# Optimization experiments

Measured on AMD Instinct MI355X. Metric: run time of the kernel, lower is better.

Reference implementation:

```python
import jax, jax.numpy as jnp
import numpy as np

NEG_SLOPE = 0.2

def gat_layer(x, src, dst, W, al, ar, b):
    # x: (N, F_in); W: (F_in, H*D); al/ar: (H, D); b: (H, D)
    N = x.shape[0]
    H, D = al.shape
    feat = (x @ W).reshape(N, H, D)                      # (N,H,D)
    el = jnp.sum(feat * al, axis=-1)                     # (N,H) src-side scores
    er = jnp.sum(feat * ar, axis=-1)                     # (N,H) dst-side scores
    e = jax.nn.leaky_relu(el[src] + er[dst], NEG_SLOPE)  # (E,H)
    # edge softmax over incoming edges of each dst node (numerically stable)
    m = jax.ops.segment_max(e, dst, num_segments=N)      # (N,H)
    m = jnp.where(jnp.isfinite(m), m, 0.0)               # guard isolated nodes
    ex = jnp.exp(e - m[dst])                             # (E,H)
    denom = jax.ops.segment_sum(ex, dst, num_segments=N) # (N,H)
    alpha = ex / jnp.maximum(denom[dst], 1e-30)          # (E,H)
    msg = alpha[:, :, None] * feat[src]                  # (E,H,D) gather + weight
    out = jax.ops.segment_sum(msg, dst, num_segments=N)  # (N,H,D) scatter-add
    return out + b[None]                                 # bias per head


def setup_inputs() -> dict:
    key = jax.random.key(0)
    ks = jax.random.split(key, 12)
    N, E, F_in, Dh = 100000, 1600000, 128, 64
    H1 = 2
    inp = {}
    inp['in_feat'] = jax.random.normal(ks[0], (N, F_in), dtype=jnp.float32)
    inp['src'] = jax.random.randint(ks[1], (E,), 0, N, dtype=jnp.int32)
    inp['dst'] = jax.random.randint(ks[2], (E,), 0, N, dtype=jnp.int32)
    s1 = 1.0 / np.sqrt(F_in)
    inp['W1'] = jax.random.normal(ks[3], (F_in, H1 * Dh), dtype=jnp.float32) * s1
    inp['al1'] = jax.random.normal(ks[4], (H1, Dh), dtype=jnp.float32) * 0.1
    inp['ar1'] = jax.random.normal(ks[5], (H1, Dh), dtype=jnp.float32) * 0.1
    inp['b1'] = jnp.zeros((H1, Dh), dtype=jnp.float32)
    s2 = 1.0 / np.sqrt(Dh)
    inp['W2'] = jax.random.normal(ks[6], (Dh, 1 * 2), dtype=jnp.float32) * s2
    inp['al2'] = jax.random.normal(ks[7], (1, 2), dtype=jnp.float32) * 0.1
    inp['ar2'] = jax.random.normal(ks[8], (1, 2), dtype=jnp.float32) * 0.1
    inp['b2'] = jnp.zeros((1, 2), dtype=jnp.float32)
    return inp


def reference(in_feat, src, dst, W1, al1, ar1, b1, W2, al2, ar2, b2):
    num_heads = al1.shape[0]
    h = gat_layer(in_feat, src, dst, W1, al1, ar1, b1)  # (N,2,64)
    h = jnp.sum(h, axis=1) / num_heads                  # head mean
    h = jax.nn.relu(h)
    out = gat_layer(h, src, dst, W2, al2, ar2, b2)      # (N,1,2)
    return out
```

## Files before the change

### kernel.cpp

```cpp
#include <hip/hip_runtime.h>
#include <hip/hip_bf16.h>
#include <hip/hip_fp16.h>

#define LEAKY 0.2f
#define NBMAX 1024
#define CCH   4096
#define SCAP2 3456

typedef _Float16 half8 __attribute__((ext_vector_type(8)));
typedef float f32x4 __attribute__((ext_vector_type(4)));

__device__ __forceinline__ float wave_sum64(float v) {
    #pragma unroll
    for (int m = 32; m > 0; m >>= 1) v += __shfl_xor(v, m, 64);
    return v;
}

__launch_bounds__(256)
__global__ void w1cvt_kernel(const float* __restrict__ W, __half* __restrict__ Wt) {
    int i = blockIdx.x * 256 + threadIdx.x;
    int n = i >> 7, k = i & 127;
    Wt[i] = __float2half(W[k * 128 + n]);
}

__launch_bounds__(256)
__global__ void gemm1_kernel(const float* __restrict__ X, const __half* __restrict__ Wt,
                             const float* __restrict__ al1, const float* __restrict__ ar1,
                             __half* __restrict__ feat_h,
                             float* __restrict__ el1, float* __restrict__ er1, int N) {
    __shared__ __half Al[64 * 136];
    __shared__ __half Wl[128 * 136];
    const int tid = threadIdx.x;
    const int r0 = blockIdx.x * 64;
    {
        int n = tid >> 1, h0 = (tid & 1) * 64;
        const __half* gsrc = Wt + n * 128 + h0;
        __half* ldst = Wl + n * 136 + h0;
        #pragma unroll
        for (int i = 0; i < 8; i++)
            *(uint4*)(ldst + i * 8) = *(const uint4*)(gsrc + i * 8);
    }
    {
        int r = tid >> 2, c0 = (tid & 3) * 32;
        int rr = r0 + r;
        const float* gsrc = X + (size_t)rr * 128 + c0;
        __half* ldst = Al + r * 136 + c0;
        if (rr < N) {
            #pragma unroll
            for (int i = 0; i < 8; i++) {
                float4 v = *(const float4*)(gsrc + i * 4);
                __half2 a = __floats2half2_rn(v.x, v.y);
                __half2 b = __floats2half2_rn(v.z, v.w);
                uint2 pk; pk.x = *(unsigned*)&a; pk.y = *(unsigned*)&b;
                *(uint2*)(ldst + i * 4) = pk;
            }
        } else {
            uint2 z; z.x = 0; z.y = 0;
            #pragma unroll
            for (int i = 0; i < 8; i++) *(uint2*)(ldst + i * 4) = z;
        }
    }
    __syncthreads();
    const int wv = tid >> 6, lane = tid & 63;
    const int lm = lane & 15, lq = lane >> 4;
    f32x4 acc[8];
    #pragma unroll
    for (int t = 0; t < 8; t++) acc[t] = (f32x4){0.f, 0.f, 0.f, 0.f};
    const __half* arow = Al + (wv * 16 + lm) * 136 + lq * 8;
    const __half* brow = Wl + lm * 136 + lq * 8;
    #pragma unroll
    for (int ks = 0; ks < 4; ks++) {
        half8 af = *(const half8*)(arow + ks * 32);
        #pragma unroll
        for (int nt = 0; nt < 8; nt++) {
            half8 bf = *(const half8*)(brow + nt * 16 * 136 + ks * 32);
            acc[nt] = __builtin_amdgcn_mfma_f32_16x16x32_f16(af, bf, acc[nt], 0, 0, 0);
        }
    }
    __syncthreads();
    __half* Cl = Al;
    #pragma unroll
    for (int nt = 0; nt < 8; nt++) {
        #pragma unroll
        for (int r = 0; r < 4; r++) {
            int m = wv * 16 + lq * 4 + r;
            Cl[m * 136 + nt * 16 + lm] = __float2half(acc[nt][r]);
        }
    }
    __syncthreads();
    {
        int r = tid >> 2, c0 = (tid & 3) * 32;
        int rr = r0 + r;
        float pel = 0.f, per = 0.f;
        const __half* crow = Cl + r * 136 + c0;
        if (rr < N) {
            #pragma unroll
            for (int i = 0; i < 4; i++)
                *(uint4*)(feat_h + (size_t)rr * 128 + c0 + i * 8) = *(const uint4*)(crow + i * 8);
            #pragma unroll
            for (int c = 0; c < 32; c++) {
                float fv = __half2float(crow[c]);
                pel += fv * al1[c0 + c];
                per += fv * ar1[c0 + c];
            }
        }
        pel += __shfl_xor(pel, 1, 64);
        per += __shfl_xor(per, 1, 64);
        if ((tid & 1) == 0 && rr < N) {
            int h = (tid >> 1) & 1;
            el1[rr * 2 + h] = pel;
            er1[rr * 2 + h] = per;
        }
    }
}

__launch_bounds__(256)
__global__ void bhist_kernel(const int* __restrict__ dst, int* __restrict__ bcount,
                             int E, int NB) {
    __shared__ int hls[NBMAX];
    for (int i = threadIdx.x; i < NB; i += 256) hls[i] = 0;
    __syncthreads();
    int stride = gridDim.x * 256;
    for (int e = blockIdx.x * 256 + threadIdx.x; e < E; e += stride)
        atomicAdd(&hls[dst[e] >> 7], 1);
    __syncthreads();
    for (int i = threadIdx.x; i < NB; i += 256) {
        int c = hls[i];
        if (c) atomicAdd(&bcount[i], c);
    }
}

__launch_bounds__(1024)
__global__ void bscan_kernel(const int* __restrict__ bcount, int* __restrict__ bstart,
                             int* __restrict__ bcursor, int NB) {
    __shared__ int sd[NBMAX];
    int t = threadIdx.x;
    int v = (t < NB) ? bcount[t] : 0;
    sd[t] = v;
    __syncthreads();
    for (int o = 1; o < NBMAX; o <<= 1) {
        int x = (t >= o) ? sd[t - o] : 0;
        __syncthreads();
        sd[t] += x;
        __syncthreads();
    }
    if (t < NB) { int ex = sd[t] - v; bstart[t] = ex; bcursor[t] = ex; }
}

__launch_bounds__(256)
__global__ void bscatter_kernel(const int* __restrict__ src, const int* __restrict__ dst,
                                const float* __restrict__ el1, const float* __restrict__ er1,
                                int* __restrict__ bcursor, uint2* __restrict__ erec,
                                int E, int NB) {
    __shared__ int hls[NBMAX];
    for (int i = threadIdx.x; i < NB; i += 256) hls[i] = 0;
    __syncthreads();
    const int b0 = blockIdx.x * CCH;
    uint2 ureg[16];
    int breg[16];
    #pragma unroll
    for (int k = 0; k < 16; k++) {
        int e = b0 + k * 256 + threadIdx.x;
        if (e < E) {
            int s = src[e], d = dst[e];
            int bk = d >> 7;
            breg[k] = bk;
            float2 lv = *((const float2*)el1 + s);
            float2 rv = *((const float2*)er1 + d);
            float e0 = lv.x + rv.x; e0 = (e0 > 0.f) ? e0 : LEAKY * e0;
            float e1 = lv.y + rv.y; e1 = (e1 > 0.f) ? e1 : LEAKY * e1;
            __half2 w = __floats2half2_rn(__expf(e0), __expf(e1));
            ureg[k].x = ((unsigned)s << 7) | (unsigned)(d & 127);
            ureg[k].y = *(unsigned*)&w;
            atomicAdd(&hls[bk], 1);
        } else breg[k] = -1;
    }
    __syncthreads();
    for (int b = threadIdx.x; b < NB; b += 256) {
        int c = hls[b];
        if (c) hls[b] = atomicAdd(&bcursor[b], c);
    }
    __syncthreads();
    #pragma unroll
    for (int k = 0; k < 16; k++) {
        if (breg[k] >= 0) {
            int p = atomicAdd(&hls[breg[k]], 1);
            erec[p] = ureg[k];
        }
    }
}

__launch_bounds__(256)
__global__ void bsort_kernel(const uint2* __restrict__ erec,
                             const int* __restrict__ bstart, const int* __restrict__ bcount,
                             uint2* __restrict__ erec2,
                             int* __restrict__ rowstart, int* __restrict__ plen,
                             int* __restrict__ tlen,
                             int N, int NB) {
    __shared__ uint2 sorted[SCAP2];
    __shared__ int cnt[128], prs[129], curs[128];
    const int tid = threadIdx.x;
    const int b = blockIdx.x;
    const int node0 = b << 7;
    const int nd = min(128, N - node0);
    const int ebase = bstart[b];
    int ecnt = bcount[b];
    if (ecnt > SCAP2 - 896) ecnt = SCAP2 - 896;
    const int pbase = ebase + 896 * b;
    if (tid < 128) cnt[tid] = 0;
    __syncthreads();
    for (int j = tid; j < ecnt; j += 256)
        atomicAdd(&cnt[erec[ebase + j].x & 127], 1);
    __syncthreads();
    int pv = 0;
    if (tid < 128) { pv = (cnt[tid] + 7) & ~7; curs[tid] = pv; }
    __syncthreads();
    for (int o = 1; o < 128; o <<= 1) {
        int x = 0;
        if (tid < 128 && tid >= o) x = curs[tid - o];
        __syncthreads();
        if (tid < 128) curs[tid] += x;
        __syncthreads();
    }
    if (tid < 128) prs[tid + 1] = curs[tid];
    if (tid == 0) prs[0] = 0;
    __syncthreads();
    if (tid < 128) curs[tid] = prs[tid + 1] - pv;
    __syncthreads();
    const int pecnt = prs[128];
    for (int j = tid; j < pecnt; j += 256) { sorted[j].x = 0; sorted[j].y = 0; }
    __syncthreads();
    for (int j = tid; j < ecnt; j += 256) {
        uint2 r = erec[ebase + j];
        int p = atomicAdd(&curs[r.x & 127], 1);
        uint2 o2;
        o2.x = (r.x >> 7) << 8;
        o2.y = r.y;
        sorted[p] = o2;
    }
    __syncthreads();
    for (int j = tid; j < pecnt; j += 256) erec2[(size_t)pbase + j] = sorted[j];
    if (tid < nd) {
        rowstart[node0 + tid] = pbase + prs[tid];
        plen[node0 + tid] = prs[tid + 1] - prs[tid];
        tlen[node0 + tid] = cnt[tid];
    }
}

__launch_bounds__(256)
__global__ void agg1_kernel(const char* __restrict__ fh, const uint2* __restrict__ erec2,
                            const float* __restrict__ b1, const float* __restrict__ W2,
                            const float* __restrict__ ar2,
                            const int* __restrict__ rowstart, const int* __restrict__ plen,
                            float* __restrict__ feat2, float* __restrict__ er2, int N) {
    int wid = (blockIdx.x * blockDim.x + threadIdx.x) >> 6;
    int lane = threadIdx.x & 63;
    if (wid >= N) return;
    const int len = plen[wid];
    const uint2* rp = erec2 + rowstart[wid];
    const int l5 = lane & 31;
    const int sub = lane >> 5;
    const unsigned hsh = (l5 < 16) ? 0u : 16u;
    float acc0 = 0.f, acc1 = 0.f, acc2 = 0.f, acc3 = 0.f, den = 0.f;
    for (int j = 0; j < len; j += 8) {
        uint2 r[4];
        #pragma unroll
        for (int u = 0; u < 4; u++) r[u] = rp[j + 2 * u + sub];
        uint2 v[4];
        #pragma unroll
        for (int u = 0; u < 4; u++)
            v[u] = *(const uint2*)(fh + (size_t)r[u].x + l5 * 8);
        #pragma unroll
        for (int u = 0; u < 4; u++) {
            float w = __half2float(__ushort_as_half((unsigned short)((r[u].y >> hsh) & 0xffffu)));
            den += w;
            float2 f0 = __half22float2(*(const __half2*)&v[u].x);
            float2 f1 = __half22float2(*(const __half2*)&v[u].y);
            acc0 += w * f0.x; acc1 += w * f0.y;
            acc2 += w * f1.x; acc3 += w * f1.y;
        }
    }
    acc0 += __shfl_xor(acc0, 32, 64);
    acc1 += __shfl_xor(acc1, 32, 64);
    acc2 += __shfl_xor(acc2, 32, 64);
    acc3 += __shfl_xor(acc3, 32, 64);
    den  += __shfl_xor(den,  32, 64);
    float inv = 1.f / fmaxf(den, 1e-30f);
    float4 bb = *(const float4*)(b1 + 4 * l5);
    float o0 = acc0 * inv + bb.x;
    float o1 = acc1 * inv + bb.y;
    float o2 = acc2 * inv + bb.z;
    float o3 = acc3 * inv + bb.w;
    float m0 = 0.5f * (o0 + __shfl_xor(o0, 16, 64));
    float m1 = 0.5f * (o1 + __shfl_xor(o1, 16, 64));
    float m2 = 0.5f * (o2 + __shfl_xor(o2, 16, 64));
    float m3 = 0.5f * (o3 + __shfl_xor(o3, 16, 64));
    m0 = fmaxf(m0, 0.f); m1 = fmaxf(m1, 0.f);
    m2 = fmaxf(m2, 0.f); m3 = fmaxf(m3, 0.f);
    const float* wrow = W2 + 8 * (l5 & 15);
    float4 wa = *(const float4*)wrow;
    float4 wb = *(const float4*)(wrow + 4);
    float p0 = m0 * wa.x + m1 * wa.z + m2 * wb.x + m3 * wb.z;
    float p1 = m0 * wa.y + m1 * wa.w + m2 * wb.y + m3 * wb.w;
    float c0 = 0.25f * wave_sum64(p0);
    float c1 = 0.25f * wave_sum64(p1);
    if (lane == 0) {
        float2 f2; f2.x = c0; f2.y = c1;
        *((float2*)feat2 + wid) = f2;
        er2[wid] = c0 * ar2[0] + c1 * ar2[1];
    }
}

__launch_bounds__(256)
__global__ void agg2_kernel(const float* __restrict__ feat2, const float* __restrict__ er2,
                            const float* __restrict__ al2, const float* __restrict__ b2,
                            const int* __restrict__ rowstart, const int* __restrict__ tlen,
                            const uint2* __restrict__ erec2, float* __restrict__ out, int N) {
    int node = (blockIdx.x * 256 + threadIdx.x) >> 4;
    int l4 = threadIdx.x & 15;
    if (node >= N) return;
    const int len = tlen[node];
    const uint2* rp = erec2 + rowstart[node];
    const float ern = er2[node];
    const float al20 = al2[0], al21 = al2[1];
    float den = 0.f, a0 = 0.f, a1 = 0.f;
    for (int j = l4; j < len; j += 16) {
        unsigned key = rp[j].x;
        float2 f = *((const float2*)feat2 + (key >> 8));
        float e = f.x * al20 + f.y * al21 + ern;
        e = (e > 0.f) ? e : LEAKY * e;
        float w = __expf(e);
        den += w;
        a0 += w * f.x;
        a1 += w * f.y;
    }
    #pragma unroll
    for (int m = 1; m < 16; m <<= 1) {
        den += __shfl_xor(den, m, 64);
        a0  += __shfl_xor(a0, m, 64);
        a1  += __shfl_xor(a1, m, 64);
    }
    if (l4 == 0) {
        float inv = 1.f / fmaxf(den, 1e-30f);
        float2 o;
        o.x = a0 * inv + b2[0];
        o.y = a1 * inv + b2[1];
        *((float2*)out + node) = o;
    }
}

extern "C" void kernel_launch(void* const* d_in, const int* in_sizes, int n_in,
                              void* d_out, int out_size, void* d_ws, size_t ws_size,
                              hipStream_t stream) {
    const float* in_feat = (const float*)d_in[0];
    const int*   src     = (const int*)d_in[1];
    const int*   dst     = (const int*)d_in[2];
    const float* W1      = (const float*)d_in[3];
    const float* al1     = (const float*)d_in[4];
    const float* ar1     = (const float*)d_in[5];
    const float* b1      = (const float*)d_in[6];
    const float* W2      = (const float*)d_in[7];
    const float* al2     = (const float*)d_in[8];
    const float* ar2     = (const float*)d_in[9];
    const float* b2      = (const float*)d_in[10];
    float* out = (float*)d_out;

    const int N = in_sizes[0] / 128;
    const int E = in_sizes[1];
    const int NB = (N + 127) >> 7;

    char* ws = (char*)d_ws;
    __half* feat1h = (__half*)ws;
    size_t off = (size_t)N * 128 * 2;
    float* el1 = (float*)(ws + off); off += (size_t)N * 2 * 4;
    float* er1 = (float*)(ws + off); off += (size_t)N * 2 * 4;
    float* feat2 = (float*)(ws + off); off += (size_t)N * 2 * 4;
    float* er2 = (float*)(ws + off); off += (size_t)N * 4;
    int* bcount  = (int*)(ws + off); off += NBMAX * 4;
    int* bstart  = (int*)(ws + off); off += NBMAX * 4;
    int* bcursor = (int*)(ws + off); off += NBMAX * 4;
    int* rowstart = (int*)(ws + off); off += (size_t)N * 4;
    int* plen     = (int*)(ws + off); off += (size_t)N * 4;
    int* tlen     = (int*)(ws + off); off += (size_t)N * 4;
    uint2* erec  = (uint2*)(ws + off); off += (size_t)E * 8;
    uint2* erec2 = (uint2*)(ws + off); off += ((size_t)E + 896 * NB) * 8;
    __half* W1t = (__half*)(ws + off); off += 128 * 128 * 2;
    (void)ws_size; (void)n_in; (void)out_size;

    hipMemsetAsync(bcount, 0, NBMAX * 4, stream);

    w1cvt_kernel<<<64, 256, 0, stream>>>(W1, W1t);
    gemm1_kernel<<<(N + 63) / 64, 256, 0, stream>>>(in_feat, W1t, al1, ar1,
                                                    feat1h, el1, er1, N);

    const int nblkC = (E + CCH - 1) / CCH;
    bhist_kernel<<<nblkC, 256, 0, stream>>>(dst, bcount, E, NB);
    bscan_kernel<<<1, 1024, 0, stream>>>(bcount, bstart, bcursor, NB);
    bscatter_kernel<<<nblkC, 256, 0, stream>>>(src, dst, el1, er1, bcursor, erec, E, NB);
    bsort_kernel<<<NB, 256, 0, stream>>>(erec, bstart, bcount, erec2, rowstart, plen, tlen, N, NB);

    agg1_kernel<<<(N * 64 + 255) / 256, 256, 0, stream>>>(
        (const char*)feat1h, erec2, b1, W2, ar2, rowstart, plen, feat2, er2, N);

    agg2_kernel<<<(N * 16 + 255) / 256, 256, 0, stream>>>(
        feat2, er2, al2, b2, rowstart, tlen, erec2, out, N);
}
```

Before: 276.1 us.

## Double-buffer edge-record and feature gathers in agg1; use fma_mix accumulation

Measured after the change: 279.4 us. Within noise of the previous version (+1.2%).

```diff
diff --git a/kernel.cpp b/kernel.cpp
--- a/kernel.cpp
+++ b/kernel.cpp
@@ -247,6 +247,21 @@
     }
 }
 
+__device__ __forceinline__ void acc_edge(uint2 r, uint2 v, unsigned hsh,
+                                         float& acc0, float& acc1,
+                                         float& acc2, float& acc3, float& den) {
+    unsigned ws = (r.y >> hsh) & 0xffffu;
+    den += __half2float(__ushort_as_half((unsigned short)ws));
+    asm("v_fma_mix_f32 %0, %1, %2, %0 op_sel:[0,0,0] op_sel_hi:[1,1,0]"
+        : "+v"(acc0) : "v"(v.x), "v"(ws));
+    asm("v_fma_mix_f32 %0, %1, %2, %0 op_sel:[1,0,0] op_sel_hi:[1,1,0]"
+        : "+v"(acc1) : "v"(v.x), "v"(ws));
+    asm("v_fma_mix_f32 %0, %1, %2, %0 op_sel:[0,0,0] op_sel_hi:[1,1,0]"
+        : "+v"(acc2) : "v"(v.y), "v"(ws));
+    asm("v_fma_mix_f32 %0, %1, %2, %0 op_sel:[1,0,0] op_sel_hi:[1,1,0]"
+        : "+v"(acc3) : "v"(v.y), "v"(ws));
+}
+
 __launch_bounds__(256)
 __global__ void agg1_kernel(const char* __restrict__ fh, const uint2* __restrict__ erec2,
                             const float* __restrict__ b1, const float* __restrict__ W2,
@@ -256,30 +271,52 @@
     int wid = (blockIdx.x * blockDim.x + threadIdx.x) >> 6;
     int lane = threadIdx.x & 63;
     if (wid >= N) return;
-    const int len = plen[wid];
-    const uint2* rp = erec2 + rowstart[wid];
+    const int len   = __builtin_amdgcn_readfirstlane(plen[wid]);
+    const int rbase = __builtin_amdgcn_readfirstlane(rowstart[wid]);
+    const uint2* __restrict__ rp = erec2 + rbase;
     const int l5 = lane & 31;
     const int sub = lane >> 5;
     const unsigned hsh = (l5 < 16) ? 0u : 16u;
+    const unsigned lofs = (unsigned)l5 * 8u;
     float acc0 = 0.f, acc1 = 0.f, acc2 = 0.f, acc3 = 0.f, den = 0.f;
-    for (int j = 0; j < len; j += 8) {
-        uint2 r[4];
-        #pragma unroll
-        for (int u = 0; u < 4; u++) r[u] = rp[j + 2 * u + sub];
-        uint2 v[4];
-        #pragma unroll
-        for (int u = 0; u < 4; u++)
-            v[u] = *(const uint2*)(fh + (size_t)r[u].x + l5 * 8);
-        #pragma unroll
-        for (int u = 0; u < 4; u++) {
-            float w = __half2float(__ushort_as_half((unsigned short)((r[u].y >> hsh) & 0xffffu)));
-            den += w;
-            float2 f0 = __half22float2(*(const __half2*)&v[u].x);
-            float2 f1 = __half22float2(*(const __half2*)&v[u].y);
-            acc0 += w * f0.x; acc1 += w * f0.y;
-            acc2 += w * f1.x; acc3 += w * f1.y;
-        }
-    }
+
+#define LDR(R, g) do { const uint2* _p = rp + ((g) * 8 + sub);                     \
+        R[0] = _p[0]; R[1] = _p[2]; R[2] = _p[4]; R[3] = _p[6]; } while (0)
+#define GTH(V, R) do {                                                             \
+        V[0] = *(const uint2*)(fh + (R[0].x + lofs));                              \
+        V[1] = *(const uint2*)(fh + (R[1].x + lofs));                              \
+        V[2] = *(const uint2*)(fh + (R[2].x + lofs));                              \
+        V[3] = *(const uint2*)(fh + (R[3].x + lofs)); } while (0)
+#define ACC(R, V) do {                                                             \
+        acc_edge(R[0], V[0], hsh, acc0, acc1, acc2, acc3, den);                    \
+        acc_edge(R[1], V[1], hsh, acc0, acc1, acc2, acc3, den);                    \
+        acc_edge(R[2], V[2], hsh, acc0, acc1, acc2, acc3, den);                    \
+        acc_edge(R[3], V[3], hsh, acc0, acc1, acc2, acc3, den); } while (0)
+
+    const int n8 = len >> 3;
+    if (n8 > 0) {
+        uint2 ra[4], rb[4], va[4], vb[4];
+        LDR(ra, 0);
+        if (n8 > 1) LDR(rb, 1);
+        GTH(va, ra);
+        int g = 0;
+        while (g + 1 < n8) {
+            GTH(vb, rb);
+            ACC(ra, va);
+            if (g + 2 < n8) LDR(ra, g + 2);
+            g++;
+            if (g + 1 >= n8) { ACC(rb, vb); g++; break; }
+            GTH(va, ra);
+            ACC(rb, vb);
+            if (g + 2 < n8) LDR(rb, g + 2);
+            g++;
+        }
+        if (g < n8) ACC(ra, va);
+    }
+#undef LDR
+#undef GTH
+#undef ACC
+
     acc0 += __shfl_xor(acc0, 32, 64);
     acc1 += __shfl_xor(acc1, 32, 64);
     acc2 += __shfl_xor(acc2, 32, 64);
```
